# Performance work log

Hardware: AMD Instinct MI355X
Metric: run time of the kernel (lower is better)

Reference implementation:

```python
import jax, jax.numpy as jnp
import numpy as np

EPS = 1e-5
PI = np.pi
HPK_SCL = 4.0  # args.hpk_scl

def _nan_to(y, rep):
    return jnp.where(jnp.isnan(y), rep, y)

def _chi(x):
    return _nan_to(1.0 / jnp.sqrt(1.0 + PI * jnp.tan(x + EPS) ** 2), 0.0)

def _E1(x, th):
    return _nan_to(jnp.exp(-(2.0 / PI) / jnp.tan(th + EPS) / jnp.tan(x + EPS)), 0.0)

def _E2(x, th):
    return _nan_to(jnp.exp(-(1.0 / PI) * (1.0 / jnp.tan(th + EPS)) ** 2 * (1.0 / jnp.tan(x + EPS)) ** 2), 0.0)

def _eta(x, th):
    y = _chi(th) * (jnp.cos(x) + jnp.sin(x) * jnp.tan(th + EPS) * (_E2(x, th) / (2.0 - _E1(x, th))))
    return _nan_to(y, 0.0)

def _f(phi):
    return _nan_to(jnp.exp(-2.0 * jnp.tan((phi + EPS) / 2.0)), 0.0)

def _mu_eff(i, e, phi, th):
    E1i, E1e = _E1(i, th), _E1(e, th)
    E2i, E2e = _E2(i, th), _E2(e, th)
    sp2 = jnp.sin(phi / 2.0) ** 2
    y1 = (E2e - sp2 * E2i) / (2.0 - E1e - phi / PI * E1i)
    y2 = (jnp.cos(phi) * E2i + sp2 * E2e) / (2.0 - E1i - phi / PI * E1e)
    y = jnp.where(i <= e, y1, y2)
    y = _chi(th) * (jnp.cos(e) + jnp.sin(e) * jnp.tan(th) * y)
    return _nan_to(y, jnp.cos(e))

def _mu0_eff(i, e, phi, th):
    E1i, E1e = _E1(i, th), _E1(e, th)
    E2i, E2e = _E2(i, th), _E2(e, th)
    sp2 = jnp.sin(phi / 2.0) ** 2
    y1 = (jnp.cos(phi) * E2e + sp2 * E2i) / (2.0 - E1e - phi / PI * E1i)
    y2 = (E2i - sp2 * E2e) / (2.0 - E1i - phi / PI * E1e)
    y = jnp.where(i <= e, y1, y2)
    y = _chi(th) * (jnp.cos(i) + jnp.sin(i) * jnp.tan(th) * y)
    return _nan_to(y, jnp.cos(i))

def _S(i, e, phi, th):
    ci, cv = jnp.cos(i), jnp.cos(e)
    mue = _mu_eff(i, e, phi, th)
    etai, etae = _eta(i, th), _eta(e, th)
    chit = _chi(th)
    ff = _f(phi)
    temp = mue / etae * (ci / etai) * chit
    y = jnp.where(i <= e,
                  temp / (1.0 - ff + ff * chit * (ci / etai)),
                  temp / (1.0 - ff + ff * chit * (cv / etae)))
    return _nan_to(y, 0.0)

def _HF(x, w):
    gamma = jnp.sqrt(1.0 - w)
    ro = (1.0 - gamma) / (1.0 + gamma)
    log = jnp.log(jnp.abs((1.0 + x) / x))
    tmp1 = 1.0 - w * x * (ro + (1.0 - 2.0 * ro * x) / 2.0 * log)
    return _nan_to(1.0 / tmp1, 1.0)

def _PF(x, b, c):
    b2 = b ** 2
    bx = b * x
    y = c * (1.0 - b2) / (jnp.power(1.0 - 2.0 * bx + b2, 1.5) + 1e-6)
    y = y + (1.0 - c) * (1.0 - b2) / (jnp.power(1.0 + 2.0 * bx + b2, 1.5) + 1e-6)
    return _nan_to(y, 0.0)

def _normalize(x):
    return x / (jnp.linalg.norm(x, axis=-1, keepdims=True) + 1e-8)

def setup_inputs() -> dict:
    N = 1048576
    key = jax.random.key(0)
    ks = jax.random.split(key, 9)
    normal = _normalize(jax.random.normal(ks[0], (N, 3), dtype=jnp.float32))
    l = _normalize(jax.random.normal(ks[1], (N, 3), dtype=jnp.float32))
    l = l * jnp.where(jnp.sum(l * normal, -1, keepdims=True) >= 0, 1.0, -1.0)  # upper hemisphere
    v = _normalize(jax.random.normal(ks[2], (N, 3), dtype=jnp.float32))
    v = v * jnp.where(jnp.sum(v * normal, -1, keepdims=True) >= 0, 1.0, -1.0)
    return {
        'pts2l': l[:, None, :],
        'pts2c': v,
        'normal': normal,
        'w': 0.05 + 0.9 * jax.random.uniform(ks[3], (N, 3), dtype=jnp.float32),
        'b': 0.8 * jax.random.uniform(ks[4], (N, 3), dtype=jnp.float32),
        'c': jax.random.uniform(ks[5], (N, 3), dtype=jnp.float32),
        'theta': 0.05 + 0.5 * jax.random.uniform(ks[6], (N,), dtype=jnp.float32),
        'h': 0.05 + 0.5 * jax.random.uniform(ks[7], (N, 1), dtype=jnp.float32),
        'B0': jax.random.uniform(ks[8], (N, 1), dtype=jnp.float32),
    }

def reference(pts2l, pts2c, normal, w, b, c, theta, h, B0):
    l = pts2l[:, 0, :]
    v = pts2c
    # angles (basic_func.calc_angles)
    ci = jnp.clip(jnp.sum(normal * l, -1), -1.0, 1.0)   # cos(incidence)
    sza = jnp.arccos(ci)
    si = jnp.sin(sza)
    cv = jnp.clip(jnp.sum(normal * v, -1), -1.0, 1.0)   # cos(view)
    vza = jnp.arccos(cv)
    sv = jnp.sin(vza)
    cg = jnp.clip(jnp.sum(l * v, -1), -1.0, 1.0)        # cos(phase)
    g = jnp.arccos(cg)
    cphi = jnp.clip((cg - ci * cv) / (si * sv + 1e-8), -1.0, 1.0)
    phi = jnp.arccos(cphi)                              # relative azimuth

    P = _PF(cg[:, None], b, c)                          # [N,3] phase function
    B = B0 / (1.0 + (1.0 / h) * jnp.tan(g / 2.0)[:, None]) + 1.0  # [N,1] opposition surge

    ci_e = _mu0_eff(sza, vza, phi, theta)               # roughness-corrected cosines
    cv_e = _mu_eff(sza, vza, phi, theta)
    Shad = _S(sza, vza, phi, theta)[:, None]            # [N,1] shadowing

    Hi = _HF(ci_e[:, None], w)                          # Chandrasekhar H functions
    Hv = _HF(cv_e[:, None], w)

    tmp1 = (ci_e / (ci_e + cv_e) / jnp.cos(sza))[:, None]
    tmp2 = P * B + Hi * Hv - 1.0
    brdf = w / HPK_SCL * tmp1 * tmp2 * Shad
    return brdf
```

## Files before the change

### kernel.cpp

```cpp
#include <hip/hip_runtime.h>


#define PIF  3.14159265358979323846f
#define EPSF 1e-5f

__device__ __forceinline__ float rcp(float x)  { return __builtin_amdgcn_rcpf(x); }
__device__ __forceinline__ float rsq(float x)  { return __builtin_amdgcn_rsqf(x); }
__device__ __forceinline__ float sqf(float x)  { return __builtin_amdgcn_sqrtf(x); }
__device__ __forceinline__ float nz(float y, float r) { return (y != y) ? r : y; }
__device__ __forceinline__ float clamp1(float x) { return fminf(fmaxf(x, -1.0f), 1.0f); }
__device__ __forceinline__ float ftan(float x) { return __sinf(x) * rcp(__cosf(x)); }

__global__ __launch_bounds__(256)
void hapke_kernel(const float* __restrict__ pts2l, const float* __restrict__ pts2c,
                  const float* __restrict__ normal, const float* __restrict__ w,
                  const float* __restrict__ b, const float* __restrict__ c,
                  const float* __restrict__ theta, const float* __restrict__ h,
                  const float* __restrict__ B0, float* __restrict__ out, int N)
{
    int idx = blockIdx.x * blockDim.x + threadIdx.x;
    if (idx >= N) return;
    const int i3 = idx * 3;

    float lx = pts2l[i3], ly = pts2l[i3+1], lz = pts2l[i3+2];
    float vx = pts2c[i3], vy = pts2c[i3+1], vz = pts2c[i3+2];
    float nx = normal[i3], ny = normal[i3+1], nzc = normal[i3+2];

    float ci = clamp1(nx*lx + ny*ly + nzc*lz);
    float cv = clamp1(nx*vx + ny*vy + nzc*vz);
    float cg = clamp1(lx*vx + ly*vy + lz*vz);
    float si = sqf(1.0f - ci*ci);
    float sv = sqf(1.0f - cv*cv);
    float cphi = clamp1((cg - ci*cv) * rcp(si*sv + 1e-8f));
    float phi  = acosf(cphi);

    float th = theta[idx];
    float t  = ftan(th + EPSF);
    float cot_th = rcp(t);
    float cot_i  = ci * rcp(si);
    float cot_e  = cv * rcp(sv);

    float E1i = nz(__expf(-(2.0f/PIF) * cot_th * cot_i), 0.0f);
    float E1e = nz(__expf(-(2.0f/PIF) * cot_th * cot_e), 0.0f);
    float ct2 = cot_th * cot_th;
    float E2i = nz(__expf(-(1.0f/PIF) * ct2 * cot_i*cot_i), 0.0f);
    float E2e = nz(__expf(-(1.0f/PIF) * ct2 * cot_e*cot_e), 0.0f);

    float chit = rsq(1.0f + PIF * t * t);
    float etai = nz(chit * (ci + si * t * (E2i * rcp(2.0f - E1i))), 0.0f);
    float etae = nz(chit * (cv + sv * t * (E2e * rcp(2.0f - E1e))), 0.0f);

    float sp2 = 0.5f * (1.0f - cphi);
    bool  ile = (ci >= cv);
    float phi_pi = phi * (1.0f / PIF);
    float rd1 = rcp(2.0f - E1e - phi_pi * E1i);
    float rd2 = rcp(2.0f - E1i - phi_pi * E1e);
    float ymu  = ile ? (E2e - sp2*E2i) * rd1 : (cphi*E2i + sp2*E2e) * rd2;
    float cv_e = nz(chit * (cv + sv * t * ymu), cv);
    float ymu0 = ile ? (cphi*E2e + sp2*E2i) * rd1 : (E2i - sp2*E2e) * rd2;
    float ci_e = nz(chit * (ci + si * t * ymu0), ci);

    float ff = __expf(-2.0f * ftan(0.5f * (phi + EPSF)));
    float ci_etai = ci * rcp(etai);
    float cv_etae = cv * rcp(etae);
    float temp = (cv_e * rcp(etae)) * ci_etai * chit;
    float shad = ile ? temp * rcp(1.0f - ff + ff * chit * ci_etai)
                     : temp * rcp(1.0f - ff + ff * chit * cv_etae);
    shad = nz(shad, 0.0f);

    float tg2 = sqf((1.0f - cg) * rcp(1.0f + cg));
    float B = B0[idx] * rcp(1.0f + rcp(h[idx]) * tg2) + 1.0f;
    float tmp1 = ci_e * rcp(ci_e + cv_e) * rcp(ci);

    float logi = __logf(fabsf((1.0f + ci_e) * rcp(ci_e)));
    float loge = __logf(fabsf((1.0f + cv_e) * rcp(cv_e)));

    #pragma unroll
    for (int k = 0; k < 3; ++k) {
        float wk = w[i3+k], bk = b[i3+k], ck = c[i3+k];
        float b2 = bk * bk;
        float bx = bk * cg;
        float t1 = 1.0f - 2.0f*bx + b2;
        float t2 = 1.0f + 2.0f*bx + b2;
        float omb2 = 1.0f - b2;
        float P = nz(ck * omb2 * rcp(t1 * sqf(t1) + 1e-6f)
                   + (1.0f - ck) * omb2 * rcp(t2 * sqf(t2) + 1e-6f), 0.0f);
        float gamma = sqf(1.0f - wk);
        float ro = (1.0f - gamma) * rcp(1.0f + gamma);
        float Hi = nz(rcp(1.0f - wk*ci_e*(ro + (1.0f - 2.0f*ro*ci_e)*0.5f*logi)), 1.0f);
        float Hv = nz(rcp(1.0f - wk*cv_e*(ro + (1.0f - 2.0f*ro*cv_e)*0.5f*loge)), 1.0f);
        float tmp2 = P * B + Hi * Hv - 1.0f;
        out[i3+k] = wk * 0.25f * tmp1 * tmp2 * shad;
    }
}

extern "C" void kernel_launch(void* const* d_in, const int* in_sizes, int n_in,
                              void* d_out, int out_size, void* d_ws, size_t ws_size,
                              hipStream_t stream) {
    const float* pts2l  = (const float*)d_in[0];
    const float* pts2c  = (const float*)d_in[1];
    const float* normal = (const float*)d_in[2];
    const float* w      = (const float*)d_in[3];
    const float* b      = (const float*)d_in[4];
    const float* c      = (const float*)d_in[5];
    const float* theta  = (const float*)d_in[6];
    const float* h      = (const float*)d_in[7];
    const float* B0     = (const float*)d_in[8];
    float* out = (float*)d_out;

    int N = in_sizes[6];
    const int block = 256;
    int grid = (N + block - 1) / block;
    hapke_kernel<<<grid, block, 0, stream>>>(pts2l, pts2c, normal, w, b, c,
                                             theta, h, B0, out, N);
}
```

Measured before the change: 124.8 us.

## Process four points per thread with float4 loads and cheaper transcendentals

```diff
diff --git a/kernel.cpp b/kernel.cpp
--- a/kernel.cpp
+++ b/kernel.cpp
@@ -9,108 +9,154 @@
 __device__ __forceinline__ float sqf(float x)  { return __builtin_amdgcn_sqrtf(x); }
 __device__ __forceinline__ float nz(float y, float r) { return (y != y) ? r : y; }
 __device__ __forceinline__ float clamp1(float x) { return fminf(fmaxf(x, -1.0f), 1.0f); }
-__device__ __forceinline__ float ftan(float x) { return __sinf(x) * rcp(__cosf(x)); }
+__device__ __forceinline__ float acos_poly(float x) {
+    float a = fabsf(x);
+    float r = sqf(1.0f - a) *
+              (1.5707288f + a * (-0.2121144f + a * (0.0742610f + a * (-0.0187293f))));
+    return (x >= 0.0f) ? r : (PIF - r);
+}
+
+#define UNPACK3(P, X, Y, Z) do { \
+    float4 _a = P[t3], _b = P[t3+1], _c = P[t3+2]; \
+    X[0]=_a.x; Y[0]=_a.y; Z[0]=_a.z;  X[1]=_a.w; Y[1]=_b.x; Z[1]=_b.y; \
+    X[2]=_b.z; Y[2]=_b.w; Z[2]=_c.x;  X[3]=_c.y; Y[3]=_c.z; Z[3]=_c.w; } while(0)
+#define UNPACK12(P, W) do { \
+    float4 _a = P[t3], _b = P[t3+1], _c = P[t3+2]; \
+    W[0]=_a.x; W[1]=_a.y; W[2]=_a.z; W[3]=_a.w; \
+    W[4]=_b.x; W[5]=_b.y; W[6]=_b.z; W[7]=_b.w; \
+    W[8]=_c.x; W[9]=_c.y; W[10]=_c.z; W[11]=_c.w; } while(0)
 
 __global__ __launch_bounds__(256)
-void hapke_kernel(const float* __restrict__ pts2l, const float* __restrict__ pts2c,
-                  const float* __restrict__ normal, const float* __restrict__ w,
-                  const float* __restrict__ b, const float* __restrict__ c,
-                  const float* __restrict__ theta, const float* __restrict__ h,
-                  const float* __restrict__ B0, float* __restrict__ out, int N)
+void hapke_kernel(const float4* __restrict__ l4, const float4* __restrict__ v4,
+                  const float4* __restrict__ n4, const float4* __restrict__ w4,
+                  const float4* __restrict__ b4, const float4* __restrict__ c4,
+                  const float4* __restrict__ th4, const float4* __restrict__ h4,
+                  const float4* __restrict__ B04, float4* __restrict__ out4, int N4)
 {
-    int idx = blockIdx.x * blockDim.x + threadIdx.x;
-    if (idx >= N) return;
-    const int i3 = idx * 3;
+    int t = blockIdx.x * blockDim.x + threadIdx.x;
+    if (t >= N4) return;
+    const int t3 = 3 * t;
 
-    float lx = pts2l[i3], ly = pts2l[i3+1], lz = pts2l[i3+2];
-    float vx = pts2c[i3], vy = pts2c[i3+1], vz = pts2c[i3+2];
-    float nx = normal[i3], ny = normal[i3+1], nzc = normal[i3+2];
+    float ci[4], cv[4], cg[4], si[4], sv[4], cphi[4], phipi[4], ff[4], tg2[4];
+    {
+        float Lx[4], Ly[4], Lz[4], Vx[4], Vy[4], Vz[4], Nx[4], Ny[4], Nz[4];
+        UNPACK3(l4, Lx, Ly, Lz);
+        UNPACK3(v4, Vx, Vy, Vz);
+        UNPACK3(n4, Nx, Ny, Nz);
+        #pragma unroll
+        for (int p = 0; p < 4; ++p) {
+            ci[p] = clamp1(Nx[p]*Lx[p] + Ny[p]*Ly[p] + Nz[p]*Lz[p]);
+            cv[p] = clamp1(Nx[p]*Vx[p] + Ny[p]*Vy[p] + Nz[p]*Vz[p]);
+            cg[p] = clamp1(Lx[p]*Vx[p] + Ly[p]*Vy[p] + Lz[p]*Vz[p]);
+            si[p] = sqf(1.0f - ci[p]*ci[p]);
+            sv[p] = sqf(1.0f - cv[p]*cv[p]);
+            float cp = clamp1((cg[p] - ci[p]*cv[p]) * rcp(si[p]*sv[p] + 1e-8f));
+            cphi[p]  = cp;
+            phipi[p] = acos_poly(cp) * (1.0f / PIF);
+            float u  = (1.0f - cp) * rcp(1.0f + cp);
+            float fv = __expf(-2.0f * sqf(u));
+            ff[p] = (cp <= -1.0f) ? __builtin_inff() : fv;
+            tg2[p] = sqf((1.0f - cg[p]) * rcp(1.0f + cg[p]));
+        }
+    }
 
-    float ci = clamp1(nx*lx + ny*ly + nzc*lz);
-    float cv = clamp1(nx*vx + ny*vy + nzc*vz);
-    float cg = clamp1(lx*vx + ly*vy + lz*vz);
-    float si = sqf(1.0f - ci*ci);
-    float sv = sqf(1.0f - cv*cv);
-    float cphi = clamp1((cg - ci*cv) * rcp(si*sv + 1e-8f));
-    float phi  = acosf(cphi);
+    float ci_e[4], cv_e[4], shad[4], tmp1[4], logi[4], loge[4];
+    {
+        float4 thv = th4[t];
+        float th[4] = {thv.x, thv.y, thv.z, thv.w};
+        #pragma unroll
+        for (int p = 0; p < 4; ++p) {
+            float s = __sinf(th[p] + EPSF), cth = __cosf(th[p] + EPSF);
+            float tt     = s * rcp(cth);
+            float cot_th = cth * rcp(s);
+            float cot_i = ci[p] * rcp(si[p]);
+            float cot_e = cv[p] * rcp(sv[p]);
+            float E1i = nz(__expf(-(2.0f/PIF) * cot_th * cot_i), 0.0f);
+            float E1e = nz(__expf(-(2.0f/PIF) * cot_th * cot_e), 0.0f);
+            float ct2 = cot_th * cot_th;
+            float E2i = nz(__expf(-(1.0f/PIF) * ct2 * cot_i*cot_i), 0.0f);
+            float E2e = nz(__expf(-(1.0f/PIF) * ct2 * cot_e*cot_e), 0.0f);
+            float chit = rsq(1.0f + PIF * tt * tt);
+            float etai = nz(chit * (ci[p] + si[p]*tt * (E2i * rcp(2.0f - E1i))), 0.0f);
+            float etae = nz(chit * (cv[p] + sv[p]*tt * (E2e * rcp(2.0f - E1e))), 0.0f);
 
-    float th = theta[idx];
-    float t  = ftan(th + EPSF);
-    float cot_th = rcp(t);
-    float cot_i  = ci * rcp(si);
-    float cot_e  = cv * rcp(sv);
+            float sp2 = 0.5f * (1.0f - cphi[p]);
+            bool ile = (ci[p] >= cv[p]);
+            float Ea  = ile ? E1e : E1i;
+            float Eb  = ile ? E1i : E1e;
+            float rd  = rcp(2.0f - Ea - phipi[p]*Eb);
+            float ymu  = (ile ? (E2e - sp2*E2i)         : (cphi[p]*E2i + sp2*E2e)) * rd;
+            float ymu0 = (ile ? (cphi[p]*E2e + sp2*E2i) : (E2i - sp2*E2e)) * rd;
+            cv_e[p] = nz(chit * (cv[p] + sv[p]*tt*ymu ), cv[p]);
+            ci_e[p] = nz(chit * (ci[p] + si[p]*tt*ymu0), ci[p]);
 
-    float E1i = nz(__expf(-(2.0f/PIF) * cot_th * cot_i), 0.0f);
-    float E1e = nz(__expf(-(2.0f/PIF) * cot_th * cot_e), 0.0f);
-    float ct2 = cot_th * cot_th;
-    float E2i = nz(__expf(-(1.0f/PIF) * ct2 * cot_i*cot_i), 0.0f);
-    float E2e = nz(__expf(-(1.0f/PIF) * ct2 * cot_e*cot_e), 0.0f);
+            float r_etai = rcp(etai), r_etae = rcp(etae);
+            float ci_etai = ci[p] * r_etai, cv_etae = cv[p] * r_etae;
+            float temp = cv_e[p] * r_etae * ci_etai * chit;
+            float den = 1.0f - ff[p] + ff[p]*chit*(ile ? ci_etai : cv_etae);
+            shad[p] = nz(temp * rcp(den), 0.0f);
 
-    float chit = rsq(1.0f + PIF * t * t);
-    float etai = nz(chit * (ci + si * t * (E2i * rcp(2.0f - E1i))), 0.0f);
-    float etae = nz(chit * (cv + sv * t * (E2e * rcp(2.0f - E1e))), 0.0f);
+            tmp1[p] = ci_e[p] * rcp((ci_e[p] + cv_e[p]) * ci[p]);
+            logi[p] = __logf(fabsf((1.0f + ci_e[p]) * rcp(ci_e[p])));
+            loge[p] = __logf(fabsf((1.0f + cv_e[p]) * rcp(cv_e[p])));
+        }
+    }
 
-    float sp2 = 0.5f * (1.0f - cphi);
-    bool  ile = (ci >= cv);
-    float phi_pi = phi * (1.0f / PIF);
-    float rd1 = rcp(2.0f - E1e - phi_pi * E1i);
-    float rd2 = rcp(2.0f - E1i - phi_pi * E1e);
-    float ymu  = ile ? (E2e - sp2*E2i) * rd1 : (cphi*E2i + sp2*E2e) * rd2;
-    float cv_e = nz(chit * (cv + sv * t * ymu), cv);
-    float ymu0 = ile ? (cphi*E2e + sp2*E2i) * rd1 : (E2i - sp2*E2e) * rd2;
-    float ci_e = nz(chit * (ci + si * t * ymu0), ci);
-
-    float ff = __expf(-2.0f * ftan(0.5f * (phi + EPSF)));
-    float ci_etai = ci * rcp(etai);
-    float cv_etae = cv * rcp(etae);
-    float temp = (cv_e * rcp(etae)) * ci_etai * chit;
-    float shad = ile ? temp * rcp(1.0f - ff + ff * chit * ci_etai)
-                     : temp * rcp(1.0f - ff + ff * chit * cv_etae);
-    shad = nz(shad, 0.0f);
-
-    float tg2 = sqf((1.0f - cg) * rcp(1.0f + cg));
-    float B = B0[idx] * rcp(1.0f + rcp(h[idx]) * tg2) + 1.0f;
-    float tmp1 = ci_e * rcp(ci_e + cv_e) * rcp(ci);
-
-    float logi = __logf(fabsf((1.0f + ci_e) * rcp(ci_e)));
-    float loge = __logf(fabsf((1.0f + cv_e) * rcp(cv_e)));
-
+    float W[12], Bb[12], Cc[12], o[12], Bv[4];
+    UNPACK12(w4, W);
+    UNPACK12(b4, Bb);
+    UNPACK12(c4, Cc);
+    {
+        float4 hv = h4[t], B0v = B04[t];
+        float hh[4] = {hv.x, hv.y, hv.z, hv.w};
+        float bb[4] = {B0v.x, B0v.y, B0v.z, B0v.w};
+        #pragma unroll
+        for (int p = 0; p < 4; ++p)
+            Bv[p] = bb[p] * hh[p] * rcp(hh[p] + tg2[p]) + 1.0f;
+    }
     #pragma unroll
-    for (int k = 0; k < 3; ++k) {
-        float wk = w[i3+k], bk = b[i3+k], ck = c[i3+k];
-        float b2 = bk * bk;
-        float bx = bk * cg;
-        float t1 = 1.0f - 2.0f*bx + b2;
-        float t2 = 1.0f + 2.0f*bx + b2;
-        float omb2 = 1.0f - b2;
-        float P = nz(ck * omb2 * rcp(t1 * sqf(t1) + 1e-6f)
-                   + (1.0f - ck) * omb2 * rcp(t2 * sqf(t2) + 1e-6f), 0.0f);
-        float gamma = sqf(1.0f - wk);
-        float ro = (1.0f - gamma) * rcp(1.0f + gamma);
-        float Hi = nz(rcp(1.0f - wk*ci_e*(ro + (1.0f - 2.0f*ro*ci_e)*0.5f*logi)), 1.0f);
-        float Hv = nz(rcp(1.0f - wk*cv_e*(ro + (1.0f - 2.0f*ro*cv_e)*0.5f*loge)), 1.0f);
-        float tmp2 = P * B + Hi * Hv - 1.0f;
-        out[i3+k] = wk * 0.25f * tmp1 * tmp2 * shad;
+    for (int p = 0; p < 4; ++p) {
+        #pragma unroll
+        for (int k = 0; k < 3; ++k) {
+            int j = 3*p + k;
+            float wk = W[j], bk = Bb[j], ck = Cc[j];
+            float b2 = bk * bk, bx = bk * cg[p];
+            float t1 = 1.0f - 2.0f*bx + b2;
+            float t2 = 1.0f + 2.0f*bx + b2;
+            float q1 = t1 * sqf(t1) + 1e-6f;
+            float q2 = t2 * sqf(t2) + 1e-6f;
+            float P = (1.0f - b2) * (ck*q2 + (1.0f - ck)*q1) * rcp(q1*q2);
+            float gamma = sqf(1.0f - wk);
+            float ro = (1.0f - gamma) * rcp(1.0f + gamma);
+            float Hi = nz(rcp(1.0f - wk*ci_e[p]*(ro + (1.0f - 2.0f*ro*ci_e[p])*0.5f*logi[p])), 1.0f);
+            float Hv = nz(rcp(1.0f - wk*cv_e[p]*(ro + (1.0f - 2.0f*ro*cv_e[p])*0.5f*loge[p])), 1.0f);
+            float tmp2 = P * Bv[p] + Hi * Hv - 1.0f;
+            o[j] = wk * 0.25f * tmp1[p] * tmp2 * shad[p];
+        }
     }
+    out4[t3]   = make_float4(o[0], o[1], o[2],  o[3]);
+    out4[t3+1] = make_float4(o[4], o[5], o[6],  o[7]);
+    out4[t3+2] = make_float4(o[8], o[9], o[10], o[11]);
 }
 
 extern "C" void kernel_launch(void* const* d_in, const int* in_sizes, int n_in,
                               void* d_out, int out_size, void* d_ws, size_t ws_size,
                               hipStream_t stream) {
-    const float* pts2l  = (const float*)d_in[0];
-    const float* pts2c  = (const float*)d_in[1];
-    const float* normal = (const float*)d_in[2];
-    const float* w      = (const float*)d_in[3];
-    const float* b      = (const float*)d_in[4];
-    const float* c      = (const float*)d_in[5];
-    const float* theta  = (const float*)d_in[6];
-    const float* h      = (const float*)d_in[7];
-    const float* B0     = (const float*)d_in[8];
-    float* out = (float*)d_out;
+    const float4* l4  = (const float4*)d_in[0];
+    const float4* v4  = (const float4*)d_in[1];
+    const float4* n4  = (const float4*)d_in[2];
+    const float4* w4  = (const float4*)d_in[3];
+    const float4* b4  = (const float4*)d_in[4];
+    const float4* c4  = (const float4*)d_in[5];
+    const float4* th4 = (const float4*)d_in[6];
+    const float4* h4  = (const float4*)d_in[7];
+    const float4* B04 = (const float4*)d_in[8];
+    float4* out4 = (float4*)d_out;
 
-    int N = in_sizes[6];
+    int N  = in_sizes[6];
+    int N4 = N >> 2;
     const int block = 256;
-    int grid = (N + block - 1) / block;
-    hapke_kernel<<<grid, block, 0, stream>>>(pts2l, pts2c, normal, w, b, c,
-                                             theta, h, B0, out, N);
+    int grid = (N4 + block - 1) / block;
+    hapke_kernel<<<grid, block, 0, stream>>>(l4, v4, n4, w4, b4, c4,
+                                             th4, h4, B04, out4, N4);
 }
```

After: 129.3 us. 3.6% more time.
